# Kernel optimization log

Hardware: AMD Instinct MI355X
Metric: run time of the kernel (lower is better)

The kernel has to match this reference:

```python
import jax, jax.numpy as jnp
import numpy as np

N_NODES = 30000; SEQ_LEN = 32; VOCAB = 10000
RNN_H = 128; RGCN_IN = 64; RGCN_H = 64; N_CLASSES = 16
N_RELS = 8; N_BASES = 4; N_EDGES = 480000


def setup_inputs() -> dict:
    key = jax.random.key(0)
    ks = jax.random.split(key, 20)
    s = 0.05
    norm = lambda k, shape: jax.random.normal(k, shape, jnp.float32) * s
    return {
        "inputs": jax.random.randint(ks[0], (N_NODES, SEQ_LEN), 0, VOCAB),
        "sequence_length": jax.random.randint(ks[1], (N_NODES,), 1, SEQ_LEN),
        "src": jax.random.randint(ks[2], (N_EDGES,), 0, N_NODES),
        "dst": jax.random.randint(ks[3], (N_EDGES,), 0, N_NODES),
        "rel_type": jax.random.randint(ks[4], (N_EDGES,), 0, N_RELS),
        "edge_norm": jax.random.uniform(ks[5], (N_EDGES,), jnp.float32),
        # RNN encoder params (only reverse-direction LSTM affects the output h_n[-1])
        "emb": norm(ks[6], (VOCAB, RNN_H)),
        "w_ih": norm(ks[7], (4 * RNN_H, RNN_H)),
        "w_hh": norm(ks[8], (4 * RNN_H, RNN_H)),
        "b_ih": norm(ks[9], (4 * RNN_H,)),
        "b_hh": norm(ks[10], (4 * RNN_H,)),
        "fc_w": norm(ks[11], (RGCN_IN, RNN_H)),
        "fc_b": norm(ks[12], (RGCN_IN,)),
        # RGCN basis-decomposed weights: W_r = sum_b w_comp[r,b] * basis[b]
        "basis0": norm(ks[13], (N_BASES, RGCN_IN, RGCN_H)),
        "wcomp0": norm(ks[14], (N_RELS, N_BASES)),
        "basis1": norm(ks[15], (N_BASES, RGCN_H, RGCN_H)),
        "wcomp1": norm(ks[16], (N_RELS, N_BASES)),
        "basis2": norm(ks[17], (N_BASES, RGCN_H, N_CLASSES)),
        "wcomp2": norm(ks[18], (N_RELS, N_BASES)),
    }


def _lstm_last(x, w_ih, w_hh, b_ih, b_hh):
    # x: [T, B, H] -> final hidden state [B, H] (PyTorch gate order: i, f, g, o)
    H = w_hh.shape[1]
    B = x.shape[1]
    h0 = jnp.zeros((B, H), x.dtype)

    def step(carry, x_t):
        h, c = carry
        z = x_t @ w_ih.T + b_ih + h @ w_hh.T + b_hh
        i, f, g, o = jnp.split(z, 4, axis=-1)
        c = jax.nn.sigmoid(f) * c + jax.nn.sigmoid(i) * jnp.tanh(g)
        h = jax.nn.sigmoid(o) * jnp.tanh(c)
        return (h, c), None

    (h, _), _ = jax.lax.scan(step, (h0, h0), x)
    return h


def _rgcn_layer(h, src, dst, rel, norm, basis, w_comp, activation):
    # Basis-decomposed RGCN: aggregate normed source feats per (dst, rel), then transform.
    # Mathematically identical to per-edge h[src] @ W[rel] scatter-summed to dst.
    n = h.shape[0]
    R = w_comp.shape[0]
    W = jnp.einsum('rb,bio->rio', w_comp, basis)            # [R, in, out]
    msg = h[src] * norm[:, None]                            # [E, in] gather
    seg = dst * R + rel                                     # scatter key (dst, rel)
    agg = jax.ops.segment_sum(msg, seg, num_segments=n * R)
    agg = agg.reshape(n, R, -1)                             # [N, R, in]
    out = jnp.einsum('nri,rio->no', agg, W)                 # [N, out]
    return activation(out) if activation is not None else out


def reference(inputs, sequence_length, src, dst, rel_type, edge_norm,
              emb, w_ih, w_hh, b_ih, b_hh, fc_w, fc_b,
              basis0, wcomp0, basis1, wcomp1, basis2, wcomp2):
    # RNN encoder: embedding -> bidirectional LSTM -> fc(h_n[-1]).
    # h_n[-1] is the reverse-direction final state, so only the reverse LSTM
    # pass affects the output; run it on the time-reversed sequence.
    x = emb[inputs.T]                                       # [T, N, H]
    h_last = _lstm_last(x[::-1], w_ih, w_hh, b_ih, b_hh)    # [N, H]
    feats = h_last @ fc_w.T + fc_b                          # [N, RGCN_IN]
    # RGCN: input/hidden layers with relu, output layer without activation.
    h = _rgcn_layer(feats, src, dst, rel_type, edge_norm, basis0, wcomp0, jax.nn.relu)
    h = _rgcn_layer(h, src, dst, rel_type, edge_norm, basis1, wcomp1, jax.nn.relu)
    h = _rgcn_layer(h, src, dst, rel_type, edge_norm, basis2, wcomp2, None)
    return h
```

## Files before the change

### kernel.cpp

```cpp
#include <hip/hip_runtime.h>

typedef float  f32x4  __attribute__((ext_vector_type(4)));
typedef short  bf16x8 __attribute__((ext_vector_type(8)));
typedef unsigned int   u32;
typedef unsigned short u16;

#define N_NODES 30000
#define VOCABSZ 10000
#define LOG2E 1.442695040888963f

__device__ __forceinline__ float sigm(float x){
  return __builtin_amdgcn_rcpf(1.f + __builtin_amdgcn_exp2f(-LOG2E*x));
}
__device__ __forceinline__ float tanh_(float x){
  return 1.f - 2.f*__builtin_amdgcn_rcpf(1.f + __builtin_amdgcn_exp2f((2.f*LOG2E)*x));
}
__device__ __forceinline__ u16 f2bf(float f){
  u32 u = __builtin_bit_cast(u32, f);
  u = u + 0x7fffu + ((u>>16)&1u);
  return (u16)(u>>16);
}
__device__ __forceinline__ float bflo(u32 u){ return __builtin_bit_cast(float, u<<16); }
__device__ __forceinline__ float bfhi(u32 u){ return __builtin_bit_cast(float, u & 0xffff0000u); }

__global__ __launch_bounds__(256) void wmat_kernel(
    const float* __restrict__ b0, const float* __restrict__ c0,
    const float* __restrict__ b1, const float* __restrict__ c1,
    const float* __restrict__ b2, const float* __restrict__ c2,
    float* __restrict__ W0, float* __restrict__ W1, float* __restrict__ W2)
{
  int id = blockIdx.x*256 + threadIdx.x;
  if (id < 32768){
    int r = id>>12;
    float s = 0.f;
    #pragma unroll
    for (int b=0;b<4;++b) s += c0[r*4+b]*b0[b*4096 + (id&4095)];
    W0[id] = s;
  } else if (id < 65536){
    int k = id - 32768;
    int r = k>>12;
    float s = 0.f;
    #pragma unroll
    for (int b=0;b<4;++b) s += c1[r*4+b]*b1[b*4096 + (k&4095)];
    W1[k] = s;
  } else if (id < 73728){
    int k = id - 65536;
    int r = k>>10;
    float s = 0.f;
    #pragma unroll
    for (int b=0;b<4;++b) s += c2[r*4+b]*b2[b*1024 + (k&1023)];
    W2[k] = s;
  }
}

__global__ __launch_bounds__(256) void embproj_kernel(
    const float* __restrict__ emb, const float* __restrict__ w_ih,
    const float* __restrict__ b_ih, const float* __restrict__ b_hh,
    u16* __restrict__ eproj)
{
  __shared__ float et[64*132];
  __shared__ float wt[32*132];
  const int tid = threadIdx.x;
  const int v0 = blockIdx.x*64;
  const int vq = tid>>4, jq = tid&15;

  for (int idx = tid*4; idx < 64*128; idx += 1024){
    int row = idx>>7, col = idx&127;
    int vr = v0 + row; if (vr > VOCABSZ-1) vr = VOCABSZ-1;
    *(f32x4*)&et[row*132+col] = *(const f32x4*)&emb[vr*128+col];
  }
  for (int jt = blockIdx.y*4; jt < blockIdx.y*4 + 4; ++jt){
    __syncthreads();
    for (int idx = tid*4; idx < 32*128; idx += 1024){
      int row = idx>>7, col = idx&127;
      *(f32x4*)&wt[row*132+col] = *(const f32x4*)&w_ih[(jt*32+row)*128+col];
    }
    __syncthreads();
    float acc[4][2] = {};
    #pragma unroll 4
    for (int k=0;k<128;++k){
      float w0v = wt[(jq*2+0)*132+k];
      float w1v = wt[(jq*2+1)*132+k];
      #pragma unroll
      for (int a=0;a<4;++a){
        float e = et[(vq*4+a)*132+k];
        acc[a][0] += e*w0v;
        acc[a][1] += e*w1v;
      }
    }
    int jb = jt*32 + jq*2;
    float bi0 = b_ih[jb]   + b_hh[jb];
    float bi1 = b_ih[jb+1] + b_hh[jb+1];
    int g  = jb>>7, rem = jb&127;
    int w  = rem>>4, q4 = (rem>>2)&3, jl = rem&3;
    int jp = w*64 + q4*16 + jl*4 + g;
    #pragma unroll
    for (int a=0;a<4;++a){
      int v = v0 + vq*4 + a;
      if (v < VOCABSZ){
        eproj[v*512 + jp]     = f2bf(acc[a][0]+bi0);
        eproj[v*512 + jp + 4] = f2bf(acc[a][1]+bi1);
      }
    }
  }
}

__global__ __launch_bounds__(512, 2) void lstm_kernel(
    const int* __restrict__ tok, const u16* __restrict__ eproj,
    const float* __restrict__ w_hh, const float* __restrict__ fc_w,
    const float* __restrict__ fc_b, float* __restrict__ feats)
{
  __shared__ __align__(16) char lds[32768];
  __shared__ u16 tokL[64*33];
  const int tid = threadIdx.x;
  const int wave = tid>>6, lane = tid&63;
  const int c16 = lane&15, g4 = lane>>4;
  const int nb = blockIdx.x*64;

  bf16x8 afr[4][4];
  #pragma unroll
  for (int g=0; g<4; ++g){
    const float* wr = w_hh + (g*128 + wave*16 + c16)*128 + g4*8;
    #pragma unroll
    for (int kk=0; kk<4; ++kk){
      f32x4 wa = *(const f32x4*)(wr + kk*32);
      f32x4 wbv = *(const f32x4*)(wr + kk*32 + 4);
      bf16x8 a;
      a[0]=(short)f2bf(wa[0]); a[1]=(short)f2bf(wa[1]);
      a[2]=(short)f2bf(wa[2]); a[3]=(short)f2bf(wa[3]);
      a[4]=(short)f2bf(wbv[0]); a[5]=(short)f2bf(wbv[1]);
      a[6]=(short)f2bf(wbv[2]); a[7]=(short)f2bf(wbv[3]);
      afr[g][kk] = a;
    }
  }
  {
    f32x4 z = {0.f,0.f,0.f,0.f};
    for (int i = tid*16; i < 16384; i += 8192) *(f32x4*)(lds + i) = z;
  }
  {
    int n = tid>>3, t0 = (tid&7)*4;
    int node = nb + n; if (node > N_NODES-1) node = N_NODES-1;
    int4 a = *(const int4*)(tok + node*32 + t0);
    tokL[n*33 + t0    ] = (u16)a.x;
    tokL[n*33 + t0 + 1] = (u16)a.y;
    tokL[n*33 + t0 + 2] = (u16)a.z;
    tokL[n*33 + t0 + 3] = (u16)a.w;
  }
  const int swz = (c16&7)<<4;
  int rb[4];
  #pragma unroll
  for (int kk=0;kk<4;++kk) rb[kk] = c16*256 + ((kk*64 + g4*16)^swz);
  const int wbB = c16*256 + ((wave*32 + g4*8)^swz);

  float creg[4][4];
  #pragma unroll
  for (int nt=0;nt<4;++nt)
    #pragma unroll
    for (int q=0;q<4;++q) creg[nt][q]=0.f;

  __syncthreads();

  const size_t gbase = (size_t)(wave*128 + g4*32);
  uint4 gxX[4], gxY[4];
  #pragma unroll
  for (int nt=0;nt<4;++nt){
    int ptok = tokL[(nt*16+c16)*33 + 31];
    const char* ep = (const char*)eproj + (size_t)ptok*1024 + gbase;
    gxX[nt] = *(const uint4*)ep;
    gxY[nt] = *(const uint4*)(ep+16);
  }

  for (int t=0; t<32; ++t){
    const int bufR = (t&1)<<14, bufW = bufR ^ 16384;
    int ptk[4];
    if (t < 31){
      #pragma unroll
      for (int nt=0;nt<4;++nt) ptk[nt] = tokL[(nt*16+c16)*33 + 30 - t];
    }
    #pragma unroll
    for (int nt=0; nt<4; ++nt){
      uint4 X = gxX[nt], Y = gxY[nt];
      f32x4 acc[4];
      acc[0][0]=bflo(X.x); acc[1][0]=bfhi(X.x); acc[2][0]=bflo(X.y); acc[3][0]=bfhi(X.y);
      acc[0][1]=bflo(X.z); acc[1][1]=bfhi(X.z); acc[2][1]=bflo(X.w); acc[3][1]=bfhi(X.w);
      acc[0][2]=bflo(Y.x); acc[1][2]=bfhi(Y.x); acc[2][2]=bflo(Y.y); acc[3][2]=bfhi(Y.y);
      acc[0][3]=bflo(Y.z); acc[1][3]=bfhi(Y.z); acc[2][3]=bflo(Y.w); acc[3][3]=bfhi(Y.w);
      if (t < 31){
        const char* ep = (const char*)eproj + (size_t)ptk[nt]*1024 + gbase;
        gxX[nt] = *(const uint4*)ep;
        gxY[nt] = *(const uint4*)(ep+16);
      }
      bf16x8 bfr[4];
      #pragma unroll
      for (int kk=0;kk<4;++kk)
        bfr[kk] = *(const bf16x8*)(lds + bufR + rb[kk] + nt*4096);
      #pragma unroll
      for (int kk=0;kk<4;++kk){
        acc[0] = __builtin_amdgcn_mfma_f32_16x16x32_bf16(afr[0][kk], bfr[kk], acc[0], 0,0,0);
        acc[1] = __builtin_amdgcn_mfma_f32_16x16x32_bf16(afr[1][kk], bfr[kk], acc[1], 0,0,0);
        acc[2] = __builtin_amdgcn_mfma_f32_16x16x32_bf16(afr[2][kk], bfr[kk], acc[2], 0,0,0);
        acc[3] = __builtin_amdgcn_mfma_f32_16x16x32_bf16(afr[3][kk], bfr[kk], acc[3], 0,0,0);
      }
      float hv[4];
      #pragma unroll
      for (int q=0;q<4;++q){
        float zi=acc[0][q], zf=acc[1][q], zg=acc[2][q], zo=acc[3][q];
        float cn = sigm(zf)*creg[nt][q] + sigm(zi)*tanh_(zg);
        creg[nt][q] = cn;
        hv[q] = sigm(zo)*tanh_(cn);
      }
      u32 plo, phi;
      asm("v_cvt_pk_bf16_f32 %0, %1, %2" : "=v"(plo) : "v"(hv[0]), "v"(hv[1]));
      asm("v_cvt_pk_bf16_f32 %0, %1, %2" : "=v"(phi) : "v"(hv[2]), "v"(hv[3]));
      uint2 hw; hw.x = plo; hw.y = phi;
      *(uint2*)(lds + bufW + wbB + nt*4096) = hw;
    }
    __syncthreads();
  }
  const int w2 = wave>>1, half = wave&1;
  f32x4 fca[2];
  #pragma unroll
  for (int oi=0;oi<2;++oi){ fca[oi][0]=0.f; fca[oi][1]=0.f; fca[oi][2]=0.f; fca[oi][3]=0.f; }
  #pragma unroll
  for (int kk=0;kk<4;++kk){
    bf16x8 b = *(const bf16x8*)(lds + rb[kk] + w2*4096);
    #pragma unroll
    for (int oi=0;oi<2;++oi){
      int ot = half*2 + oi;
      const float* fr = fc_w + (ot*16 + c16)*128 + kk*32 + g4*8;
      f32x4 wa = *(const f32x4*)fr;
      f32x4 wbv = *(const f32x4*)(fr+4);
      bf16x8 a;
      a[0]=(short)f2bf(wa[0]); a[1]=(short)f2bf(wa[1]);
      a[2]=(short)f2bf(wa[2]); a[3]=(short)f2bf(wa[3]);
      a[4]=(short)f2bf(wbv[0]); a[5]=(short)f2bf(wbv[1]);
      a[6]=(short)f2bf(wbv[2]); a[7]=(short)f2bf(wbv[3]);
      fca[oi] = __builtin_amdgcn_mfma_f32_16x16x32_bf16(a, b, fca[oi], 0,0,0);
    }
  }
  const int node = nb + w2*16 + c16;
  if (node < N_NODES){
    #pragma unroll
    for (int oi=0;oi<2;++oi)
      #pragma unroll
      for (int q=0;q<4;++q){
        int o = (half*2+oi)*16 + g4*4 + q;
        feats[node*64 + o] = fca[oi][q] + fc_b[o];
      }
  }
}

template<int NO, bool RELU>
__global__ __launch_bounds__(256) void transform_kernel(
    const float* __restrict__ h, const float* __restrict__ W,
    float* __restrict__ tmp, int n_nodes)
{
  __shared__ float As[64][68];
  __shared__ float Bs[64][132];
  const int tid = threadIdx.x;
  const int n0 = blockIdx.x*64;
  const int j0 = blockIdx.y*128;
  constexpr int WIDTH = 8*NO;

  for (int idx = tid*4; idx < 4096; idx += 1024){
    int r = idx>>6, c = idx&63;
    int n = n0 + r; if (n > n_nodes-1) n = n_nodes-1;
    f32x4 v = *(const f32x4*)(h + (size_t)n*64 + c);
    if (RELU){
      v[0]=fmaxf(v[0],0.f); v[1]=fmaxf(v[1],0.f);
      v[2]=fmaxf(v[2],0.f); v[3]=fmaxf(v[3],0.f);
    }
    *(f32x4*)&As[r][c] = v;
  }
  for (int idx = tid*4; idx < 8192; idx += 1024){
    int k = idx>>7, j = idx&127;
    int jj = j0 + j;
    int r = jj / NO, o = jj & (NO-1);
    f32x4 v = *(const f32x4*)(W + r*(64*NO) + k*NO + o);
    *(f32x4*)&Bs[k][j] = v;
  }
  __syncthreads();

  const int tx = tid&15, ty = tid>>4;
  float acc[4][8];
  #pragma unroll
  for (int i=0;i<4;++i)
    #pragma unroll
    for (int j=0;j<8;++j) acc[i][j]=0.f;

  #pragma unroll 4
  for (int k=0;k<64;++k){
    f32x4 b0 = *(const f32x4*)&Bs[k][tx*8];
    f32x4 b1 = *(const f32x4*)&Bs[k][tx*8+4];
    #pragma unroll
    for (int i=0;i<4;++i){
      float a = As[ty*4+i][k];
      #pragma unroll
      for (int j=0;j<4;++j){
        acc[i][j]   += a*b0[j];
        acc[i][j+4] += a*b1[j];
      }
    }
  }
  #pragma unroll
  for (int i=0;i<4;++i){
    int n = n0 + ty*4 + i;
    if (n < n_nodes){
      *(f32x4*)(tmp + (size_t)n*WIDTH + j0 + tx*8)     = *(f32x4*)&acc[i][0];
      *(f32x4*)(tmp + (size_t)n*WIDTH + j0 + tx*8 + 4) = *(f32x4*)&acc[i][4];
    }
  }
}

template<int NO>
__global__ __launch_bounds__(256) void scatter_kernel(
    const float* __restrict__ tmp, const int* __restrict__ src,
    const int* __restrict__ dst, const int* __restrict__ rel,
    const float* __restrict__ enorm, float* __restrict__ out, int n_edges)
{
  constexpr int EPW = 64/NO;
  constexpr int WIDTH = 8*NO;
  const int lane = threadIdx.x & 63;
  const int es = (NO==64) ? 0 : (lane>>4);
  const int o  = lane & (NO-1);
  const long gw = (long)((blockIdx.x*256 + threadIdx.x)>>6);
  const long stride = (long)gridDim.x*4*EPW;
  long e = gw*EPW + es;
  if (e >= n_edges) return;
  int s=src[e], d=dst[e], r=rel[e]; float nm=enorm[e];
  float v = tmp[(size_t)s*WIDTH + r*NO + o];
  while (true){
    long e1 = e + stride;
    bool more = (e1 < n_edges);
    int s1=0,d1=0,r1=0; float nm1=0.f, v1=0.f;
    if (more){
      s1=src[e1]; d1=dst[e1]; r1=rel[e1]; nm1=enorm[e1];
      v1 = tmp[(size_t)s1*WIDTH + r1*NO + o];
    }
    unsafeAtomicAdd(out + (size_t)d*NO + o, v*nm);
    if (!more) break;
    s=s1; d=d1; r=r1; nm=nm1; v=v1; e=e1;
  }
}

extern "C" void kernel_launch(void* const* d_in, const int* in_sizes, int n_in,
                              void* d_out, int out_size, void* d_ws, size_t ws_size,
                              hipStream_t stream)
{
  const int*   tok    = (const int*)  d_in[0];
  const int*   src    = (const int*)  d_in[2];
  const int*   dst    = (const int*)  d_in[3];
  const int*   rel    = (const int*)  d_in[4];
  const float* enorm  = (const float*)d_in[5];
  const float* emb    = (const float*)d_in[6];
  const float* w_ih   = (const float*)d_in[7];
  const float* w_hh   = (const float*)d_in[8];
  const float* b_ih   = (const float*)d_in[9];
  const float* b_hh   = (const float*)d_in[10];
  const float* fc_w   = (const float*)d_in[11];
  const float* fc_b   = (const float*)d_in[12];
  const float* basis0 = (const float*)d_in[13];
  const float* wcomp0 = (const float*)d_in[14];
  const float* basis1 = (const float*)d_in[15];
  const float* wcomp1 = (const float*)d_in[16];
  const float* basis2 = (const float*)d_in[17];
  const float* wcomp2 = (const float*)d_in[18];

  char* ws = (char*)d_ws;
  float* tmp   = (float*)(ws);
  u16*   eproj = (u16*)  (ws);
  float* feats = (float*)(ws + 61440000);
  float* g1    = (float*)(ws + 69120000);
  float* g2    = (float*)(ws + 76800000);
  float* W0    = (float*)(ws + 84480000);
  float* W1    = (float*)(ws + 84611072);
  float* W2    = (float*)(ws + 84742144);

  wmat_kernel<<<288, 256, 0, stream>>>(basis0, wcomp0, basis1, wcomp1,
                                       basis2, wcomp2, W0, W1, W2);
  embproj_kernel<<<dim3(157,4), 256, 0, stream>>>(emb, w_ih, b_ih, b_hh, eproj);

  hipMemsetAsync(g1, 0, 15360000, stream);
  hipMemsetAsync(d_out, 0, 30000*16*4, stream);

  lstm_kernel<<<469, 512, 0, stream>>>(tok, eproj, w_hh, fc_w, fc_b, feats);

  transform_kernel<64,false><<<dim3(469,4), 256, 0, stream>>>(feats, W0, tmp, N_NODES);
  scatter_kernel<64><<<2048, 256, 0, stream>>>(tmp, src, dst, rel, enorm, g1, 480000);

  transform_kernel<64,true><<<dim3(469,4), 256, 0, stream>>>(g1, W1, tmp, N_NODES);
  scatter_kernel<64><<<2048, 256, 0, stream>>>(tmp, src, dst, rel, enorm, g2, 480000);

  transform_kernel<16,true><<<dim3(469,1), 256, 0, stream>>>(g2, W2, tmp, N_NODES);
  scatter_kernel<16><<<2048, 256, 0, stream>>>(tmp, src, dst, rel, enorm, (float*)d_out, 480000);
}
```

Before: 685.4 us.

## Fuse input projection into LSTM and replace atomic scatter with CSR gather

Drops the precomputed per-vocab gate projection table and instead stages bf16 embeddings into LDS each timestep, computing W_ih·x with extra MFMAs alongside W_hh·h. This cuts per-token gather traffic from a 1KB projection row to a 256B embedding row at the cost of doubling MFMA work. Separately, edges are sorted by destination via histogram/scan/permute kernels, and each RGCN aggregation becomes a per-node gather without atomics or zeroing memsets. This adds a CSR build each call.

```diff
diff --git a/kernel.cpp b/kernel.cpp
--- a/kernel.cpp
+++ b/kernel.cpp
@@ -6,6 +6,7 @@
 typedef unsigned short u16;
 
 #define N_NODES 30000
+#define N_EDGES 480000
 #define VOCABSZ 10000
 #define LOG2E 1.442695040888963f
 
@@ -20,8 +21,6 @@
   u = u + 0x7fffu + ((u>>16)&1u);
   return (u16)(u>>16);
 }
-__device__ __forceinline__ float bflo(u32 u){ return __builtin_bit_cast(float, u<<16); }
-__device__ __forceinline__ float bfhi(u32 u){ return __builtin_bit_cast(float, u & 0xffff0000u); }
 
 __global__ __launch_bounds__(256) void wmat_kernel(
     const float* __restrict__ b0, const float* __restrict__ c0,
@@ -53,86 +52,67 @@
   }
 }
 
-__global__ __launch_bounds__(256) void embproj_kernel(
-    const float* __restrict__ emb, const float* __restrict__ w_ih,
+__global__ __launch_bounds__(256) void ebf_kernel(
+    const float* __restrict__ emb, u16* __restrict__ ebf)
+{
+  int id = blockIdx.x*256 + threadIdx.x;
+  if (id < 320000){
+    f32x4 v = *(const f32x4*)(emb + (size_t)id*4);
+    u16 o0 = f2bf(v[0]), o1 = f2bf(v[1]), o2 = f2bf(v[2]), o3 = f2bf(v[3]);
+    u32 lo = (u32)o0 | ((u32)o1<<16);
+    u32 hi = (u32)o2 | ((u32)o3<<16);
+    uint2 pk; pk.x = lo; pk.y = hi;
+    *(uint2*)(ebf + (size_t)id*4) = pk;
+  }
+}
+
+__global__ __launch_bounds__(512, 2) void lstm_kernel(
+    const int* __restrict__ tok, const u16* __restrict__ ebf,
+    const float* __restrict__ w_ih, const float* __restrict__ w_hh,
     const float* __restrict__ b_ih, const float* __restrict__ b_hh,
-    u16* __restrict__ eproj)
-{
-  __shared__ float et[64*132];
-  __shared__ float wt[32*132];
-  const int tid = threadIdx.x;
-  const int v0 = blockIdx.x*64;
-  const int vq = tid>>4, jq = tid&15;
-
-  for (int idx = tid*4; idx < 64*128; idx += 1024){
-    int row = idx>>7, col = idx&127;
-    int vr = v0 + row; if (vr > VOCABSZ-1) vr = VOCABSZ-1;
-    *(f32x4*)&et[row*132+col] = *(const f32x4*)&emb[vr*128+col];
-  }
-  for (int jt = blockIdx.y*4; jt < blockIdx.y*4 + 4; ++jt){
-    __syncthreads();
-    for (int idx = tid*4; idx < 32*128; idx += 1024){
-      int row = idx>>7, col = idx&127;
-      *(f32x4*)&wt[row*132+col] = *(const f32x4*)&w_ih[(jt*32+row)*128+col];
-    }
-    __syncthreads();
-    float acc[4][2] = {};
-    #pragma unroll 4
-    for (int k=0;k<128;++k){
-      float w0v = wt[(jq*2+0)*132+k];
-      float w1v = wt[(jq*2+1)*132+k];
-      #pragma unroll
-      for (int a=0;a<4;++a){
-        float e = et[(vq*4+a)*132+k];
-        acc[a][0] += e*w0v;
-        acc[a][1] += e*w1v;
-      }
-    }
-    int jb = jt*32 + jq*2;
-    float bi0 = b_ih[jb]   + b_hh[jb];
-    float bi1 = b_ih[jb+1] + b_hh[jb+1];
-    int g  = jb>>7, rem = jb&127;
-    int w  = rem>>4, q4 = (rem>>2)&3, jl = rem&3;
-    int jp = w*64 + q4*16 + jl*4 + g;
-    #pragma unroll
-    for (int a=0;a<4;++a){
-      int v = v0 + vq*4 + a;
-      if (v < VOCABSZ){
-        eproj[v*512 + jp]     = f2bf(acc[a][0]+bi0);
-        eproj[v*512 + jp + 4] = f2bf(acc[a][1]+bi1);
-      }
-    }
-  }
-}
-
-__global__ __launch_bounds__(512, 2) void lstm_kernel(
-    const int* __restrict__ tok, const u16* __restrict__ eproj,
-    const float* __restrict__ w_hh, const float* __restrict__ fc_w,
-    const float* __restrict__ fc_b, float* __restrict__ feats)
+    const float* __restrict__ fc_w, const float* __restrict__ fc_b,
+    float* __restrict__ feats)
 {
   __shared__ __align__(16) char lds[32768];
+  __shared__ __align__(16) char xld[32768];
   __shared__ u16 tokL[64*33];
   const int tid = threadIdx.x;
   const int wave = tid>>6, lane = tid&63;
   const int c16 = lane&15, g4 = lane>>4;
   const int nb = blockIdx.x*64;
 
-  bf16x8 afr[4][4];
+  bf16x8 ahh[4][4], aih[4][4];
   #pragma unroll
   for (int g=0; g<4; ++g){
-    const float* wr = w_hh + (g*128 + wave*16 + c16)*128 + g4*8;
+    const float* wrh = w_hh + (g*128 + wave*16 + c16)*128 + g4*8;
+    const float* wri = w_ih + (g*128 + wave*16 + c16)*128 + g4*8;
     #pragma unroll
     for (int kk=0; kk<4; ++kk){
-      f32x4 wa = *(const f32x4*)(wr + kk*32);
-      f32x4 wbv = *(const f32x4*)(wr + kk*32 + 4);
-      bf16x8 a;
-      a[0]=(short)f2bf(wa[0]); a[1]=(short)f2bf(wa[1]);
-      a[2]=(short)f2bf(wa[2]); a[3]=(short)f2bf(wa[3]);
-      a[4]=(short)f2bf(wbv[0]); a[5]=(short)f2bf(wbv[1]);
-      a[6]=(short)f2bf(wbv[2]); a[7]=(short)f2bf(wbv[3]);
-      afr[g][kk] = a;
-    }
-  }
+      f32x4 ha = *(const f32x4*)(wrh + kk*32);
+      f32x4 hb = *(const f32x4*)(wrh + kk*32 + 4);
+      f32x4 ia = *(const f32x4*)(wri + kk*32);
+      f32x4 ib = *(const f32x4*)(wri + kk*32 + 4);
+      bf16x8 a, b;
+      a[0]=(short)f2bf(ha[0]); a[1]=(short)f2bf(ha[1]);
+      a[2]=(short)f2bf(ha[2]); a[3]=(short)f2bf(ha[3]);
+      a[4]=(short)f2bf(hb[0]); a[5]=(short)f2bf(hb[1]);
+      a[6]=(short)f2bf(hb[2]); a[7]=(short)f2bf(hb[3]);
+      b[0]=(short)f2bf(ia[0]); b[1]=(short)f2bf(ia[1]);
+      b[2]=(short)f2bf(ia[2]); b[3]=(short)f2bf(ia[3]);
+      b[4]=(short)f2bf(ib[0]); b[5]=(short)f2bf(ib[1]);
+      b[6]=(short)f2bf(ib[2]); b[7]=(short)f2bf(ib[3]);
+      ahh[g][kk] = a; aih[g][kk] = b;
+    }
+  }
+  float bias[4][4];
+  #pragma unroll
+  for (int g=0; g<4; ++g)
+    #pragma unroll
+    for (int q=0; q<4; ++q){
+      int j = g*128 + wave*16 + g4*4 + q;
+      bias[g][q] = b_ih[j] + b_hh[j];
+    }
+
   {
     f32x4 z = {0.f,0.f,0.f,0.f};
     for (int i = tid*16; i < 16384; i += 8192) *(f32x4*)(lds + i) = z;
@@ -146,6 +126,21 @@
     tokL[n*33 + t0 + 2] = (u16)a.z;
     tokL[n*33 + t0 + 3] = (u16)a.w;
   }
+  __syncthreads();
+
+  const int srow = tid>>3, sseg = tid&7;
+  const int sx0 = srow*256 + ((sseg*32)    ^ ((srow&7)<<4));
+  const int sx1 = srow*256 + ((sseg*32+16) ^ ((srow&7)<<4));
+
+  {
+    int tk = tokL[srow*33 + 31];
+    const char* ep = (const char*)ebf + (size_t)tk*256 + sseg*32;
+    uint4 a = *(const uint4*)ep;
+    uint4 b = *(const uint4*)(ep+16);
+    *(uint4*)(xld + sx0) = a;
+    *(uint4*)(xld + sx1) = b;
+  }
+
   const int swz = (c16&7)<<4;
   int rb[4];
   #pragma unroll
@@ -160,51 +155,47 @@
 
   __syncthreads();
 
-  const size_t gbase = (size_t)(wave*128 + g4*32);
-  uint4 gxX[4], gxY[4];
-  #pragma unroll
-  for (int nt=0;nt<4;++nt){
-    int ptok = tokL[(nt*16+c16)*33 + 31];
-    const char* ep = (const char*)eproj + (size_t)ptok*1024 + gbase;
-    gxX[nt] = *(const uint4*)ep;
-    gxY[nt] = *(const uint4*)(ep+16);
-  }
-
   for (int t=0; t<32; ++t){
     const int bufR = (t&1)<<14, bufW = bufR ^ 16384;
-    int ptk[4];
+    char* xcur = xld + ((t&1)<<14);
+    char* xnxt = xld + (((t+1)&1)<<14);
+    uint4 sa, sb;
     if (t < 31){
-      #pragma unroll
-      for (int nt=0;nt<4;++nt) ptk[nt] = tokL[(nt*16+c16)*33 + 30 - t];
+      int tk = tokL[srow*33 + 30 - t];
+      const char* ep = (const char*)ebf + (size_t)tk*256 + sseg*32;
+      sa = *(const uint4*)ep;
+      sb = *(const uint4*)(ep+16);
     }
     #pragma unroll
     for (int nt=0; nt<4; ++nt){
-      uint4 X = gxX[nt], Y = gxY[nt];
+      bf16x8 bfr[4], bx[4];
+      #pragma unroll
+      for (int kk=0;kk<4;++kk){
+        bfr[kk] = *(const bf16x8*)(lds + bufR + rb[kk] + nt*4096);
+        bx[kk]  = *(const bf16x8*)(xcur + rb[kk] + nt*4096);
+      }
       f32x4 acc[4];
-      acc[0][0]=bflo(X.x); acc[1][0]=bfhi(X.x); acc[2][0]=bflo(X.y); acc[3][0]=bfhi(X.y);
-      acc[0][1]=bflo(X.z); acc[1][1]=bfhi(X.z); acc[2][1]=bflo(X.w); acc[3][1]=bfhi(X.w);
-      acc[0][2]=bflo(Y.x); acc[1][2]=bfhi(Y.x); acc[2][2]=bflo(Y.y); acc[3][2]=bfhi(Y.y);
-      acc[0][3]=bflo(Y.z); acc[1][3]=bfhi(Y.z); acc[2][3]=bflo(Y.w); acc[3][3]=bfhi(Y.w);
-      if (t < 31){
-        const char* ep = (const char*)eproj + (size_t)ptk[nt]*1024 + gbase;
-        gxX[nt] = *(const uint4*)ep;
-        gxY[nt] = *(const uint4*)(ep+16);
-      }
-      bf16x8 bfr[4];
-      #pragma unroll
-      for (int kk=0;kk<4;++kk)
-        bfr[kk] = *(const bf16x8*)(lds + bufR + rb[kk] + nt*4096);
+      #pragma unroll
+      for (int g=0;g<4;++g){ acc[g][0]=0.f; acc[g][1]=0.f; acc[g][2]=0.f; acc[g][3]=0.f; }
       #pragma unroll
       for (int kk=0;kk<4;++kk){
-        acc[0] = __builtin_amdgcn_mfma_f32_16x16x32_bf16(afr[0][kk], bfr[kk], acc[0], 0,0,0);
-        acc[1] = __builtin_amdgcn_mfma_f32_16x16x32_bf16(afr[1][kk], bfr[kk], acc[1], 0,0,0);
-        acc[2] = __builtin_amdgcn_mfma_f32_16x16x32_bf16(afr[2][kk], bfr[kk], acc[2], 0,0,0);
-        acc[3] = __builtin_amdgcn_mfma_f32_16x16x32_bf16(afr[3][kk], bfr[kk], acc[3], 0,0,0);
+        acc[0] = __builtin_amdgcn_mfma_f32_16x16x32_bf16(ahh[0][kk], bfr[kk], acc[0], 0,0,0);
+        acc[1] = __builtin_amdgcn_mfma_f32_16x16x32_bf16(ahh[1][kk], bfr[kk], acc[1], 0,0,0);
+        acc[2] = __builtin_amdgcn_mfma_f32_16x16x32_bf16(ahh[2][kk], bfr[kk], acc[2], 0,0,0);
+        acc[3] = __builtin_amdgcn_mfma_f32_16x16x32_bf16(ahh[3][kk], bfr[kk], acc[3], 0,0,0);
+      }
+      #pragma unroll
+      for (int kk=0;kk<4;++kk){
+        acc[0] = __builtin_amdgcn_mfma_f32_16x16x32_bf16(aih[0][kk], bx[kk], acc[0], 0,0,0);
+        acc[1] = __builtin_amdgcn_mfma_f32_16x16x32_bf16(aih[1][kk], bx[kk], acc[1], 0,0,0);
+        acc[2] = __builtin_amdgcn_mfma_f32_16x16x32_bf16(aih[2][kk], bx[kk], acc[2], 0,0,0);
+        acc[3] = __builtin_amdgcn_mfma_f32_16x16x32_bf16(aih[3][kk], bx[kk], acc[3], 0,0,0);
       }
       float hv[4];
       #pragma unroll
       for (int q=0;q<4;++q){
-        float zi=acc[0][q], zf=acc[1][q], zg=acc[2][q], zo=acc[3][q];
+        float zi=acc[0][q]+bias[0][q], zf=acc[1][q]+bias[1][q];
+        float zg=acc[2][q]+bias[2][q], zo=acc[3][q]+bias[3][q];
         float cn = sigm(zf)*creg[nt][q] + sigm(zi)*tanh_(zg);
         creg[nt][q] = cn;
         hv[q] = sigm(zo)*tanh_(cn);
@@ -214,6 +205,10 @@
       asm("v_cvt_pk_bf16_f32 %0, %1, %2" : "=v"(phi) : "v"(hv[2]), "v"(hv[3]));
       uint2 hw; hw.x = plo; hw.y = phi;
       *(uint2*)(lds + bufW + wbB + nt*4096) = hw;
+    }
+    if (t < 31){
+      *(uint4*)(xnxt + sx0) = sa;
+      *(uint4*)(xnxt + sx1) = sb;
     }
     __syncthreads();
   }
@@ -250,6 +245,57 @@
   }
 }
 
+__global__ __launch_bounds__(256) void hist_kernel(
+    const int* __restrict__ dst, int* __restrict__ cnt, int n)
+{
+  int e = blockIdx.x*256 + threadIdx.x;
+  if (e < n) atomicAdd(&cnt[dst[e]], 1);
+}
+
+__global__ __launch_bounds__(1024) void scan_kernel(
+    int* __restrict__ cnt, int* __restrict__ ofs)
+{
+  __shared__ int sums[1024];
+  const int tid = threadIdx.x;
+  const int base = tid*30;
+  int loc[30]; int s = 0;
+  #pragma unroll
+  for (int i=0;i<30;++i){
+    int d = base + i;
+    int c = (d < N_NODES) ? cnt[d] : 0;
+    loc[i] = s; s += c;
+  }
+  sums[tid] = s;
+  __syncthreads();
+  for (int off=1; off<1024; off<<=1){
+    int v = (tid >= off) ? sums[tid-off] : 0;
+    __syncthreads();
+    sums[tid] += v;
+    __syncthreads();
+  }
+  int excl = sums[tid] - s;
+  #pragma unroll
+  for (int i=0;i<30;++i){
+    int d = base + i;
+    if (d <= N_NODES){
+      int v = excl + loc[i];
+      ofs[d] = v;
+      if (d < N_NODES) cnt[d] = v;
+    }
+  }
+}
+
+__global__ __launch_bounds__(256) void permute_kernel(
+    const int* __restrict__ dst, int* __restrict__ cur,
+    int* __restrict__ perm, int n)
+{
+  int e = blockIdx.x*256 + threadIdx.x;
+  if (e < n){
+    int p = atomicAdd(&cur[dst[e]], 1);
+    perm[p] = e;
+  }
+}
+
 template<int NO, bool RELU>
 __global__ __launch_bounds__(256) void transform_kernel(
     const float* __restrict__ h, const float* __restrict__ W,
@@ -313,34 +359,37 @@
 }
 
 template<int NO>
-__global__ __launch_bounds__(256) void scatter_kernel(
-    const float* __restrict__ tmp, const int* __restrict__ src,
-    const int* __restrict__ dst, const int* __restrict__ rel,
-    const float* __restrict__ enorm, float* __restrict__ out, int n_edges)
-{
-  constexpr int EPW = 64/NO;
+__global__ __launch_bounds__(256) void gather_kernel(
+    const float* __restrict__ tmp, const int* __restrict__ perm,
+    const int* __restrict__ ofs, const int* __restrict__ src,
+    const int* __restrict__ rel, const float* __restrict__ enorm,
+    float* __restrict__ out)
+{
   constexpr int WIDTH = 8*NO;
   const int lane = threadIdx.x & 63;
-  const int es = (NO==64) ? 0 : (lane>>4);
-  const int o  = lane & (NO-1);
-  const long gw = (long)((blockIdx.x*256 + threadIdx.x)>>6);
-  const long stride = (long)gridDim.x*4*EPW;
-  long e = gw*EPW + es;
-  if (e >= n_edges) return;
-  int s=src[e], d=dst[e], r=rel[e]; float nm=enorm[e];
-  float v = tmp[(size_t)s*WIDTH + r*NO + o];
-  while (true){
-    long e1 = e + stride;
-    bool more = (e1 < n_edges);
-    int s1=0,d1=0,r1=0; float nm1=0.f, v1=0.f;
-    if (more){
-      s1=src[e1]; d1=dst[e1]; r1=rel[e1]; nm1=enorm[e1];
-      v1 = tmp[(size_t)s1*WIDTH + r1*NO + o];
-    }
-    unsafeAtomicAdd(out + (size_t)d*NO + o, v*nm);
-    if (!more) break;
-    s=s1; d=d1; r=r1; nm=nm1; v=v1; e=e1;
-  }
+  const int wid = (blockIdx.x*256 + threadIdx.x) >> 6;
+  int d, o;
+  if (NO == 64){ d = wid; o = lane; }
+  else         { d = wid*4 + (lane>>4); o = lane & 15; }
+  if (d >= N_NODES) return;
+  const int beg = ofs[d], end = ofs[d+1];
+  float acc = 0.f;
+  if (beg < end){
+    int pe = perm[beg];
+    int s = src[pe], r = rel[pe]; float nm = enorm[pe];
+    for (int i = beg; i < end; ){
+      float v = tmp[(size_t)s*WIDTH + r*NO + o];
+      ++i;
+      int s1=0, r1=0; float nm1=0.f;
+      if (i < end){
+        int pe1 = perm[i];
+        s1 = src[pe1]; r1 = rel[pe1]; nm1 = enorm[pe1];
+      }
+      acc += nm * v;
+      s = s1; r = r1; nm = nm1;
+    }
+  }
+  out[(size_t)d*NO + o] = acc;
 }
 
 extern "C" void kernel_launch(void* const* d_in, const int* in_sizes, int n_in,
@@ -368,8 +417,11 @@
 
   char* ws = (char*)d_ws;
   float* tmp   = (float*)(ws);
-  u16*   eproj = (u16*)  (ws);
+  u16*   ebf   = (u16*)  (ws);
   float* feats = (float*)(ws + 61440000);
+  int*   ofs   = (int*)  (ws + 61440000);
+  int*   cur   = (int*)  (ws + 61560064);
+  int*   perm  = (int*)  (ws + 61680128);
   float* g1    = (float*)(ws + 69120000);
   float* g2    = (float*)(ws + 76800000);
   float* W0    = (float*)(ws + 84480000);
@@ -378,19 +430,22 @@
 
   wmat_kernel<<<288, 256, 0, stream>>>(basis0, wcomp0, basis1, wcomp1,
                                        basis2, wcomp2, W0, W1, W2);
-  embproj_kernel<<<dim3(157,4), 256, 0, stream>>>(emb, w_ih, b_ih, b_hh, eproj);
-
-  hipMemsetAsync(g1, 0, 15360000, stream);
-  hipMemsetAsync(d_out, 0, 30000*16*4, stream);
-
-  lstm_kernel<<<469, 512, 0, stream>>>(tok, eproj, w_hh, fc_w, fc_b, feats);
+  ebf_kernel<<<1250, 256, 0, stream>>>(emb, ebf);
+  lstm_kernel<<<469, 512, 0, stream>>>(tok, ebf, w_ih, w_hh, b_ih, b_hh,
+                                       fc_w, fc_b, feats);
 
   transform_kernel<64,false><<<dim3(469,4), 256, 0, stream>>>(feats, W0, tmp, N_NODES);
-  scatter_kernel<64><<<2048, 256, 0, stream>>>(tmp, src, dst, rel, enorm, g1, 480000);
+
+  hipMemsetAsync(cur, 0, 120004, stream);
+  hist_kernel<<<1875, 256, 0, stream>>>(dst, cur, N_EDGES);
+  scan_kernel<<<1, 1024, 0, stream>>>(cur, ofs);
+  permute_kernel<<<1875, 256, 0, stream>>>(dst, cur, perm, N_EDGES);
+
+  gather_kernel<64><<<7500, 256, 0, stream>>>(tmp, perm, ofs, src, rel, enorm, g1);
 
   transform_kernel<64,true><<<dim3(469,4), 256, 0, stream>>>(g1, W1, tmp, N_NODES);
-  scatter_kernel<64><<<2048, 256, 0, stream>>>(tmp, src, dst, rel, enorm, g2, 480000);
+  gather_kernel<64><<<7500, 256, 0, stream>>>(tmp, perm, ofs, src, rel, enorm, g2);
 
   transform_kernel<16,true><<<dim3(469,1), 256, 0, stream>>>(g2, W2, tmp, N_NODES);
-  scatter_kernel<16><<<2048, 256, 0, stream>>>(tmp, src, dst, rel, enorm, (float*)d_out, 480000);
-}
+  gather_kernel<16><<<1875, 256, 0, stream>>>(tmp, perm, ofs, src, rel, enorm, (float*)d_out);
+}
```

After: 750.0 us. 1.09x slower.

## Replace atomic scatter with CSR gather aggregation and shrink LSTM blocks

Applied to the files above, without the earlier changes.

Builds a destination-sorted edge index (histogram, single-block scan, atomic permutation) and replaces the atomic-add scatter in each RGCN layer with a per-destination gather that writes outputs directly, removing atomics and output memsets. The LSTM kernel now processes 32 nodes per block with a higher occupancy hint to raise concurrency. The CSR build adds extra launches and a serial one-block scan, and the gather relies on indirect perm/src/rel loads.

```diff
diff --git a/kernel.cpp b/kernel.cpp
--- a/kernel.cpp
+++ b/kernel.cpp
@@ -6,6 +6,7 @@
 typedef unsigned short u16;
 
 #define N_NODES 30000
+#define N_EDGES 480000
 #define VOCABSZ 10000
 #define LOG2E 1.442695040888963f
 
@@ -105,17 +106,17 @@
   }
 }
 
-__global__ __launch_bounds__(512, 2) void lstm_kernel(
+__global__ __launch_bounds__(512, 4) void lstm_kernel(
     const int* __restrict__ tok, const u16* __restrict__ eproj,
     const float* __restrict__ w_hh, const float* __restrict__ fc_w,
     const float* __restrict__ fc_b, float* __restrict__ feats)
 {
-  __shared__ __align__(16) char lds[32768];
-  __shared__ u16 tokL[64*33];
+  __shared__ __align__(16) char lds[16384];
+  __shared__ u16 tokL[32*33];
   const int tid = threadIdx.x;
   const int wave = tid>>6, lane = tid&63;
   const int c16 = lane&15, g4 = lane>>4;
-  const int nb = blockIdx.x*64;
+  const int nb = blockIdx.x*32;
 
   bf16x8 afr[4][4];
   #pragma unroll
@@ -135,9 +136,9 @@
   }
   {
     f32x4 z = {0.f,0.f,0.f,0.f};
-    for (int i = tid*16; i < 16384; i += 8192) *(f32x4*)(lds + i) = z;
-  }
-  {
+    *(f32x4*)(lds + tid*16) = z;
+  }
+  if (tid < 256){
     int n = tid>>3, t0 = (tid&7)*4;
     int node = nb + n; if (node > N_NODES-1) node = N_NODES-1;
     int4 a = *(const int4*)(tok + node*32 + t0);
@@ -152,18 +153,18 @@
   for (int kk=0;kk<4;++kk) rb[kk] = c16*256 + ((kk*64 + g4*16)^swz);
   const int wbB = c16*256 + ((wave*32 + g4*8)^swz);
 
-  float creg[4][4];
-  #pragma unroll
-  for (int nt=0;nt<4;++nt)
+  float creg[2][4];
+  #pragma unroll
+  for (int nt=0;nt<2;++nt)
     #pragma unroll
     for (int q=0;q<4;++q) creg[nt][q]=0.f;
 
   __syncthreads();
 
   const size_t gbase = (size_t)(wave*128 + g4*32);
-  uint4 gxX[4], gxY[4];
-  #pragma unroll
-  for (int nt=0;nt<4;++nt){
+  uint4 gxX[2], gxY[2];
+  #pragma unroll
+  for (int nt=0;nt<2;++nt){
     int ptok = tokL[(nt*16+c16)*33 + 31];
     const char* ep = (const char*)eproj + (size_t)ptok*1024 + gbase;
     gxX[nt] = *(const uint4*)ep;
@@ -171,14 +172,9 @@
   }
 
   for (int t=0; t<32; ++t){
-    const int bufR = (t&1)<<14, bufW = bufR ^ 16384;
-    int ptk[4];
-    if (t < 31){
-      #pragma unroll
-      for (int nt=0;nt<4;++nt) ptk[nt] = tokL[(nt*16+c16)*33 + 30 - t];
-    }
-    #pragma unroll
-    for (int nt=0; nt<4; ++nt){
+    const int bufR = (t&1)<<13, bufW = bufR ^ 8192;
+    #pragma unroll
+    for (int nt=0; nt<2; ++nt){
       uint4 X = gxX[nt], Y = gxY[nt];
       f32x4 acc[4];
       acc[0][0]=bflo(X.x); acc[1][0]=bfhi(X.x); acc[2][0]=bflo(X.y); acc[3][0]=bfhi(X.y);
@@ -186,20 +182,18 @@
       acc[0][2]=bflo(Y.x); acc[1][2]=bfhi(Y.x); acc[2][2]=bflo(Y.y); acc[3][2]=bfhi(Y.y);
       acc[0][3]=bflo(Y.z); acc[1][3]=bfhi(Y.z); acc[2][3]=bflo(Y.w); acc[3][3]=bfhi(Y.w);
       if (t < 31){
-        const char* ep = (const char*)eproj + (size_t)ptk[nt]*1024 + gbase;
+        int ptok = tokL[(nt*16+c16)*33 + 30 - t];
+        const char* ep = (const char*)eproj + (size_t)ptok*1024 + gbase;
         gxX[nt] = *(const uint4*)ep;
         gxY[nt] = *(const uint4*)(ep+16);
       }
-      bf16x8 bfr[4];
-      #pragma unroll
-      for (int kk=0;kk<4;++kk)
-        bfr[kk] = *(const bf16x8*)(lds + bufR + rb[kk] + nt*4096);
       #pragma unroll
       for (int kk=0;kk<4;++kk){
-        acc[0] = __builtin_amdgcn_mfma_f32_16x16x32_bf16(afr[0][kk], bfr[kk], acc[0], 0,0,0);
-        acc[1] = __builtin_amdgcn_mfma_f32_16x16x32_bf16(afr[1][kk], bfr[kk], acc[1], 0,0,0);
-        acc[2] = __builtin_amdgcn_mfma_f32_16x16x32_bf16(afr[2][kk], bfr[kk], acc[2], 0,0,0);
-        acc[3] = __builtin_amdgcn_mfma_f32_16x16x32_bf16(afr[3][kk], bfr[kk], acc[3], 0,0,0);
+        bf16x8 b = *(const bf16x8*)(lds + bufR + rb[kk] + nt*4096);
+        acc[0] = __builtin_amdgcn_mfma_f32_16x16x32_bf16(afr[0][kk], b, acc[0], 0,0,0);
+        acc[1] = __builtin_amdgcn_mfma_f32_16x16x32_bf16(afr[1][kk], b, acc[1], 0,0,0);
+        acc[2] = __builtin_amdgcn_mfma_f32_16x16x32_bf16(afr[2][kk], b, acc[2], 0,0,0);
+        acc[3] = __builtin_amdgcn_mfma_f32_16x16x32_bf16(afr[3][kk], b, acc[3], 0,0,0);
       }
       float hv[4];
       #pragma unroll
@@ -217,36 +211,80 @@
     }
     __syncthreads();
   }
-  const int w2 = wave>>1, half = wave&1;
-  f32x4 fca[2];
-  #pragma unroll
-  for (int oi=0;oi<2;++oi){ fca[oi][0]=0.f; fca[oi][1]=0.f; fca[oi][2]=0.f; fca[oi][3]=0.f; }
+  const int ntE = wave>>2, ot = wave&3;
+  f32x4 fca;
+  fca[0]=0.f; fca[1]=0.f; fca[2]=0.f; fca[3]=0.f;
   #pragma unroll
   for (int kk=0;kk<4;++kk){
-    bf16x8 b = *(const bf16x8*)(lds + rb[kk] + w2*4096);
-    #pragma unroll
-    for (int oi=0;oi<2;++oi){
-      int ot = half*2 + oi;
-      const float* fr = fc_w + (ot*16 + c16)*128 + kk*32 + g4*8;
-      f32x4 wa = *(const f32x4*)fr;
-      f32x4 wbv = *(const f32x4*)(fr+4);
-      bf16x8 a;
-      a[0]=(short)f2bf(wa[0]); a[1]=(short)f2bf(wa[1]);
-      a[2]=(short)f2bf(wa[2]); a[3]=(short)f2bf(wa[3]);
-      a[4]=(short)f2bf(wbv[0]); a[5]=(short)f2bf(wbv[1]);
-      a[6]=(short)f2bf(wbv[2]); a[7]=(short)f2bf(wbv[3]);
-      fca[oi] = __builtin_amdgcn_mfma_f32_16x16x32_bf16(a, b, fca[oi], 0,0,0);
-    }
-  }
-  const int node = nb + w2*16 + c16;
+    bf16x8 b = *(const bf16x8*)(lds + rb[kk] + ntE*4096);
+    const float* fr = fc_w + (ot*16 + c16)*128 + kk*32 + g4*8;
+    f32x4 wa = *(const f32x4*)fr;
+    f32x4 wbv = *(const f32x4*)(fr+4);
+    bf16x8 a;
+    a[0]=(short)f2bf(wa[0]); a[1]=(short)f2bf(wa[1]);
+    a[2]=(short)f2bf(wa[2]); a[3]=(short)f2bf(wa[3]);
+    a[4]=(short)f2bf(wbv[0]); a[5]=(short)f2bf(wbv[1]);
+    a[6]=(short)f2bf(wbv[2]); a[7]=(short)f2bf(wbv[3]);
+    fca = __builtin_amdgcn_mfma_f32_16x16x32_bf16(a, b, fca, 0,0,0);
+  }
+  const int node = nb + ntE*16 + c16;
   if (node < N_NODES){
     #pragma unroll
-    for (int oi=0;oi<2;++oi)
-      #pragma unroll
-      for (int q=0;q<4;++q){
-        int o = (half*2+oi)*16 + g4*4 + q;
-        feats[node*64 + o] = fca[oi][q] + fc_b[o];
-      }
+    for (int q=0;q<4;++q){
+      int o = ot*16 + g4*4 + q;
+      feats[node*64 + o] = fca[q] + fc_b[o];
+    }
+  }
+}
+
+__global__ __launch_bounds__(256) void hist_kernel(
+    const int* __restrict__ dst, int* __restrict__ cnt, int n)
+{
+  int e = blockIdx.x*256 + threadIdx.x;
+  if (e < n) atomicAdd(&cnt[dst[e]], 1);
+}
+
+__global__ __launch_bounds__(1024) void scan_kernel(
+    int* __restrict__ cnt, int* __restrict__ ofs)
+{
+  __shared__ int sums[1024];
+  const int tid = threadIdx.x;
+  const int base = tid*30;
+  int loc[30]; int s = 0;
+  #pragma unroll
+  for (int i=0;i<30;++i){
+    int d = base + i;
+    int c = (d < N_NODES) ? cnt[d] : 0;
+    loc[i] = s; s += c;
+  }
+  sums[tid] = s;
+  __syncthreads();
+  for (int off=1; off<1024; off<<=1){
+    int v = (tid >= off) ? sums[tid-off] : 0;
+    __syncthreads();
+    sums[tid] += v;
+    __syncthreads();
+  }
+  int excl = sums[tid] - s;
+  #pragma unroll
+  for (int i=0;i<30;++i){
+    int d = base + i;
+    if (d <= N_NODES){
+      int v = excl + loc[i];
+      ofs[d] = v;
+      if (d < N_NODES) cnt[d] = v;
+    }
+  }
+}
+
+__global__ __launch_bounds__(256) void permute_kernel(
+    const int* __restrict__ dst, int* __restrict__ cur,
+    int* __restrict__ perm, int n)
+{
+  int e = blockIdx.x*256 + threadIdx.x;
+  if (e < n){
+    int p = atomicAdd(&cur[dst[e]], 1);
+    perm[p] = e;
   }
 }
 
@@ -313,34 +351,37 @@
 }
 
 template<int NO>
-__global__ __launch_bounds__(256) void scatter_kernel(
-    const float* __restrict__ tmp, const int* __restrict__ src,
-    const int* __restrict__ dst, const int* __restrict__ rel,
-    const float* __restrict__ enorm, float* __restrict__ out, int n_edges)
-{
-  constexpr int EPW = 64/NO;
+__global__ __launch_bounds__(256) void gather_kernel(
+    const float* __restrict__ tmp, const int* __restrict__ perm,
+    const int* __restrict__ ofs, const int* __restrict__ src,
+    const int* __restrict__ rel, const float* __restrict__ enorm,
+    float* __restrict__ out)
+{
   constexpr int WIDTH = 8*NO;
   const int lane = threadIdx.x & 63;
-  const int es = (NO==64) ? 0 : (lane>>4);
-  const int o  = lane & (NO-1);
-  const long gw = (long)((blockIdx.x*256 + threadIdx.x)>>6);
-  const long stride = (long)gridDim.x*4*EPW;
-  long e = gw*EPW + es;
-  if (e >= n_edges) return;
-  int s=src[e], d=dst[e], r=rel[e]; float nm=enorm[e];
-  float v = tmp[(size_t)s*WIDTH + r*NO + o];
-  while (true){
-    long e1 = e + stride;
-    bool more = (e1 < n_edges);
-    int s1=0,d1=0,r1=0; float nm1=0.f, v1=0.f;
-    if (more){
-      s1=src[e1]; d1=dst[e1]; r1=rel[e1]; nm1=enorm[e1];
-      v1 = tmp[(size_t)s1*WIDTH + r1*NO + o];
-    }
-    unsafeAtomicAdd(out + (size_t)d*NO + o, v*nm);
-    if (!more) break;
-    s=s1; d=d1; r=r1; nm=nm1; v=v1; e=e1;
-  }
+  const int wid = (blockIdx.x*256 + threadIdx.x) >> 6;
+  int d, o;
+  if (NO == 64){ d = wid; o = lane; }
+  else         { d = wid*4 + (lane>>4); o = lane & 15; }
+  if (d >= N_NODES) return;
+  const int beg = ofs[d], end = ofs[d+1];
+  float acc = 0.f;
+  if (beg < end){
+    int pe = perm[beg];
+    int s = src[pe], r = rel[pe]; float nm = enorm[pe];
+    for (int i = beg; i < end; ){
+      float v = tmp[(size_t)s*WIDTH + r*NO + o];
+      ++i;
+      int s1=0, r1=0; float nm1=0.f;
+      if (i < end){
+        int pe1 = perm[i];
+        s1 = src[pe1]; r1 = rel[pe1]; nm1 = enorm[pe1];
+      }
+      acc += nm * v;
+      s = s1; r = r1; nm = nm1;
+    }
+  }
+  out[(size_t)d*NO + o] = acc;
 }
 
 extern "C" void kernel_launch(void* const* d_in, const int* in_sizes, int n_in,
@@ -370,6 +411,9 @@
   float* tmp   = (float*)(ws);
   u16*   eproj = (u16*)  (ws);
   float* feats = (float*)(ws + 61440000);
+  int*   ofs   = (int*)  (ws + 61440000);
+  int*   cur   = (int*)  (ws + 61560064);
+  int*   perm  = (int*)  (ws + 61680128);
   float* g1    = (float*)(ws + 69120000);
   float* g2    = (float*)(ws + 76800000);
   float* W0    = (float*)(ws + 84480000);
@@ -379,18 +423,20 @@
   wmat_kernel<<<288, 256, 0, stream>>>(basis0, wcomp0, basis1, wcomp1,
                                        basis2, wcomp2, W0, W1, W2);
   embproj_kernel<<<dim3(157,4), 256, 0, stream>>>(emb, w_ih, b_ih, b_hh, eproj);
-
-  hipMemsetAsync(g1, 0, 15360000, stream);
-  hipMemsetAsync(d_out, 0, 30000*16*4, stream);
-
-  lstm_kernel<<<469, 512, 0, stream>>>(tok, eproj, w_hh, fc_w, fc_b, feats);
+  lstm_kernel<<<938, 512, 0, stream>>>(tok, eproj, w_hh, fc_w, fc_b, feats);
 
   transform_kernel<64,false><<<dim3(469,4), 256, 0, stream>>>(feats, W0, tmp, N_NODES);
-  scatter_kernel<64><<<2048, 256, 0, stream>>>(tmp, src, dst, rel, enorm, g1, 480000);
+
+  hipMemsetAsync(cur, 0, 120004, stream);
+  hist_kernel<<<1875, 256, 0, stream>>>(dst, cur, N_EDGES);
+  scan_kernel<<<1, 1024, 0, stream>>>(cur, ofs);
+  permute_kernel<<<1875, 256, 0, stream>>>(dst, cur, perm, N_EDGES);
+
+  gather_kernel<64><<<7500, 256, 0, stream>>>(tmp, perm, ofs, src, rel, enorm, g1);
 
   transform_kernel<64,true><<<dim3(469,4), 256, 0, stream>>>(g1, W1, tmp, N_NODES);
-  scatter_kernel<64><<<2048, 256, 0, stream>>>(tmp, src, dst, rel, enorm, g2, 480000);
+  gather_kernel<64><<<7500, 256, 0, stream>>>(tmp, perm, ofs, src, rel, enorm, g2);
 
   transform_kernel<16,true><<<dim3(469,1), 256, 0, stream>>>(g2, W2, tmp, N_NODES);
-  scatter_kernel<16><<<2048, 256, 0, stream>>>(tmp, src, dst, rel, enorm, (float*)d_out, 480000);
-}
+  gather_kernel<16><<<1875, 256, 0, stream>>>(tmp, perm, ofs, src, rel, enorm, (float*)d_out);
+}
```

New measurement: 700.3 us. 2.2% more time.
